# Kernel optimization log

Hardware: AMD Instinct MI355X
Metric: run time of the kernel (lower is better)

The kernel has to match this reference:

```python
import jax, jax.numpy as jnp
import numpy as np

NTRIAL, NNEUR, NT, NT_FULL, NTAU, NLAT, NPAD = 8, 100, 256, 300, 50, 8, 44
LR, JITTER, ZERO_THRESH = 0.2, 1e-3, 1e-5


def setup_inputs() -> dict:
    key = jax.random.key(0)
    k1, k2, k3, k4 = jax.random.split(key, 4)
    Y = jax.random.uniform(k1, (NTRIAL, NNEUR, NT), dtype=jnp.float32)
    raw_input = jax.random.uniform(k2, (NTRIAL, NNEUR, NT_FULL), dtype=jnp.float32)
    kernel = 0.05 * jax.random.normal(k3, (NNEUR, NTAU, NNEUR), dtype=jnp.float32)
    readout = 0.02 * jax.random.normal(k4, (NNEUR, NLAT), dtype=jnp.float32)
    t = jnp.arange(NT, dtype=jnp.float32)
    K = jnp.exp(-(t[:, None] - t[None, :]) ** 2 / (2.0 * 20.0 ** 2))  # RBF latent covariance
    bias = jnp.zeros((), jnp.float32)
    return {"Y": Y, "raw_input": raw_input, "kernel": kernel, "readout": readout,
            "K": K, "bias": bias, "max_iter": 5}


def _conv(raw_input, kernel, npadding):
    # raw_input: (m, i, nt_full); kernel: (i, ntau, j)
    ntrial, ni, nt = raw_input.shape
    zero_pad = jnp.zeros((kernel.shape[0], 1, kernel.shape[2]), kernel.dtype)
    kernel = jnp.concatenate([zero_pad, kernel], axis=1)  # enforce causality
    ntau = kernel.shape[1]
    nn = nt + ntau - 1
    Fx = jnp.fft.fft(raw_input, n=nn, axis=2)[:, :, :, None]   # (m, i, nn, 1)
    Fk = jnp.fft.fft(kernel, n=nn, axis=1)[None]                # (1, i, nn, j)
    G = jnp.fft.ifft(Fx * Fk, axis=2).real
    G = jnp.where(jnp.abs(G) < ZERO_THRESH, 0.0, G)
    G = G[:, :, npadding:nt, :]                                 # (m, i, t, j)
    return jnp.transpose(G, (0, 1, 3, 2)).astype(raw_input.dtype)  # (m, i, j, t)


def _gpfa_poisson_fix_weights(Y, weights, K, bias, max_iter):
    # Y: (m, n, t); weights: (m, n, l, t); K: (t, t)
    ntrial, nneuron, nlatent, nt = weights.shape
    I = jnp.eye(nt, dtype=K.dtype)
    inv_K = jnp.linalg.inv(K + JITTER * I)
    w2 = weights ** 2
    mu0 = jnp.zeros((ntrial, nlatent, nt), K.dtype)
    hess0 = jnp.broadcast_to(inv_K, (ntrial, nlatent, nt, nt)) + jnp.zeros((ntrial, nlatent, 1, 1), K.dtype)

    def step(carry, _):
        mu, hessian, _, _ = carry
        log_lambd = jnp.einsum('mnlt,mlt->mnt', weights, mu) + bias
        hinv = jnp.linalg.inv(hessian)                              # (m, l, t, t)
        dhinv = jnp.diagonal(hinv, axis1=-2, axis2=-1)              # (m, l, t)
        lambd = jnp.exp(log_lambd + 0.5 * jnp.einsum('mlt,mnlt->mnt', dhinv, w2))
        iKh = jnp.einsum('tu,mluv->mltv', inv_K, hinv)              # inv_K @ hessian^{-1}
        muK = jnp.einsum('mlt,tu->mlu', mu, inv_K)
        _, logabs = jnp.linalg.slogdet(iKh)
        loss = (jnp.sum(Y * log_lambd) - jnp.sum(lambd)
                - 0.5 * jnp.sum(muK * mu)
                - 0.5 * jnp.sum(jnp.trace(iKh, axis1=-2, axis2=-1))
                + 0.5 * jnp.sum(logabs) - nt)
        grad = jnp.einsum('mnlt,mnt->mlt', weights, Y - lambd) - muK
        w2l = jnp.einsum('mnlt,mnt->mlt', w2, lambd)                # (m, l, t)
        new_h = -inv_K[None, None] - w2l[..., None] * I             # 4D diagonal add
        mu_upd = jnp.linalg.solve(new_h, grad[..., None])[..., 0]
        return (mu - LR * mu_upd, new_h, lambd, loss), None

    carry0 = (mu0, hess0, jnp.zeros_like(Y), jnp.zeros((), K.dtype))
    (mu, hessian, lambd, loss), _ = jax.lax.scan(step, carry0, None, length=max_iter)
    return mu, lambd, loss


def reference(Y, raw_input, kernel, readout, K, bias, max_iter):
    G = _conv(raw_input, kernel, NPAD)                       # (m, i, j, t)
    weights = jnp.einsum('mijt,il->mjlt', G, readout)        # (m, n=j, l, t)
    mu, lambd, loss = _gpfa_poisson_fix_weights(Y, weights, K, bias, max_iter)
    return mu, lambd, loss
```

## Files before the change

kernel.cpp:

```cpp
#include <hip/hip_runtime.h>

#define NTRIAL 8
#define NNEUR 100
#define NTT 256
#define NT_FULL 300
#define NTAU 50
#define NLAT 8
#define NPAD 44
#define LRATE 0.2f
#define JITTER 0.001f
#define NMAT 64
#define NSLOT 136
#define SPITCH 260
#define NBLKF 35360
#define NBLKF4 8840

__device__ __forceinline__ int bslot(int I, int J){ return ((I*(I+1))>>1) + J; }
__device__ __forceinline__ int rcs(int i, int j){
    return i*16 + ((((j>>2) + (i>>2))&3)<<2) + (j&3);
}
__device__ __forceinline__ int eidx(int I, int J, int i, int j){
    return bslot(I,J)*SPITCH + rcs(i,j);
}
__device__ __forceinline__ int rc4(int i, int q){ return i*4 + ((q + (i>>2))&3); }
__device__ __forceinline__ int f4idx(int I, int J, int i, int q){
    return bslot(I,J)*65 + rc4(i,q);
}
#define DOT4(u,v) (u.x*v.x + u.y*v.y + u.z*v.z + u.w*v.w)

__device__ __forceinline__ void gemmRR(const float4* A, int baseA, const float4* B, int baseB,
                                       int ti, int tj, float acc[4][4]){
    #pragma unroll
    for (int kc = 0; kc < 4; ++kc){
        float4 a0 = A[baseA + rc4(ti+0,kc)];
        float4 a1 = A[baseA + rc4(ti+1,kc)];
        float4 a2 = A[baseA + rc4(ti+2,kc)];
        float4 a3 = A[baseA + rc4(ti+3,kc)];
        float4 b0 = B[baseB + rc4(tj+0,kc)];
        float4 b1 = B[baseB + rc4(tj+1,kc)];
        float4 b2 = B[baseB + rc4(tj+2,kc)];
        float4 b3 = B[baseB + rc4(tj+3,kc)];
        acc[0][0]+=DOT4(a0,b0); acc[0][1]+=DOT4(a0,b1); acc[0][2]+=DOT4(a0,b2); acc[0][3]+=DOT4(a0,b3);
        acc[1][0]+=DOT4(a1,b0); acc[1][1]+=DOT4(a1,b1); acc[1][2]+=DOT4(a1,b2); acc[1][3]+=DOT4(a1,b3);
        acc[2][0]+=DOT4(a2,b0); acc[2][1]+=DOT4(a2,b1); acc[2][2]+=DOT4(a2,b2); acc[2][3]+=DOT4(a2,b3);
        acc[3][0]+=DOT4(a3,b0); acc[3][1]+=DOT4(a3,b1); acc[3][2]+=DOT4(a3,b2); acc[3][3]+=DOT4(a3,b3);
    }
}

__global__ void k_zero(float* mu, float* scal){
    int i = blockIdx.x*256 + threadIdx.x;
    if (i < 16384) mu[i] = 0.f;
    if (i < 64) scal[i] = 0.f;
}

__global__ void k_transpose(const float* __restrict__ kern, float* __restrict__ kt){
    int idx = blockIdx.x*256 + threadIdx.x;
    if (idx >= NNEUR*NTAU*NNEUR) return;
    int i = idx/(NTAU*NNEUR); int rem = idx%(NTAU*NNEUR);
    int tau = rem/NNEUR; int j = rem%NNEUR;
    kt[((size_t)i*NNEUR + j)*NTAU + tau] = kern[idx];
}

__global__ __launch_bounds__(256) void k_conv_weights(const float* __restrict__ raw,
                                                      const float* __restrict__ kt,
                                                      const float* __restrict__ readout,
                                                      float* __restrict__ W){
    int b = blockIdx.x; int m = b / NNEUR; int j = b % NNEUR; int t = threadIdx.x;
    __shared__ float ro[NNEUR*NLAT];
    __shared__ float raw_s[10][NT_FULL];
    __shared__ float kern_s[10][NTAU];
    for (int idx = t; idx < NNEUR*NLAT; idx += 256) ro[idx] = readout[idx];
    float acc[NLAT];
    #pragma unroll
    for (int l = 0; l < NLAT; ++l) acc[l] = 0.f;
    int tmax = min(NTAU, t + NPAD);
    for (int c = 0; c < 10; ++c){
        __syncthreads();
        for (int idx = t; idx < 10*NT_FULL; idx += 256){
            int ii = idx / NT_FULL, tt = idx % NT_FULL;
            raw_s[ii][tt] = raw[((size_t)m*NNEUR + c*10 + ii)*NT_FULL + tt];
        }
        for (int idx = t; idx < 10*NTAU; idx += 256){
            int ii = idx / NTAU, tau = idx % NTAU;
            kern_s[ii][tau] = kt[((size_t)(c*10 + ii)*NNEUR + j)*NTAU + tau];
        }
        __syncthreads();
        for (int ii = 0; ii < 10; ++ii){
            float g = 0.f;
            const float* kr = kern_s[ii];
            const float* rr = raw_s[ii];
            for (int tau = 1; tau <= tmax; ++tau) g += kr[tau-1] * rr[t + NPAD - tau];
            if (fabsf(g) < 1e-5f) g = 0.f;
            const float* rop = &ro[(c*10 + ii)*NLAT];
            #pragma unroll
            for (int l = 0; l < NLAT; ++l) acc[l] += rop[l]*g;
        }
    }
    #pragma unroll
    for (int l = 0; l < NLAT; ++l) W[(((size_t)b)*NLAT + l)*NTT + t] = acc[l];
}

__global__ __launch_bounds__(256) void k_grad2(const float* __restrict__ W, const float* __restrict__ Y,
                                               const float* __restrict__ bias_p,
                                               const float* __restrict__ muIn, const float* __restrict__ diagIn,
                                               float* __restrict__ gradPart, float* __restrict__ w2lPart,
                                               float* __restrict__ lambd, float* __restrict__ scal,
                                               int it0, int it4){
    int blk = blockIdx.x; int m = blk >> 3; int chunk = blk & 7;
    int n0 = chunk*12 + (chunk < 4 ? chunk : 4);
    int cnt = 12 + (chunk < 4 ? 1 : 0);
    int t = threadIdx.x;
    __shared__ float r1[256], r2[256];
    float mul[NLAT], dhl[NLAT];
    #pragma unroll
    for (int l = 0; l < NLAT; ++l){
        mul[l] = muIn[((size_t)(m*NLAT + l))*NTT + t];
        dhl[l] = it0 ? (1.0f + JITTER) : (-diagIn[((size_t)(m*NLAT + l))*NTT + t]);
    }
    float bias = bias_p[0];
    float ga[NLAT], wa[NLAT];
    #pragma unroll
    for (int l = 0; l < NLAT; ++l){ ga[l] = 0.f; wa[l] = 0.f; }
    float yl = 0.f, ls = 0.f;
    for (int n = n0; n < n0 + cnt; ++n){
        size_t base = (((size_t)(m*NNEUR + n))*NLAT)*NTT + t;
        float wl[NLAT];
        float ll = bias, q = 0.f;
        #pragma unroll
        for (int l = 0; l < NLAT; ++l){
            float w = W[base + (size_t)l*NTT];
            wl[l] = w;
            ll += w * mul[l];
            q  += w * w * dhl[l];
        }
        float lam = expf(ll + 0.5f*q);
        float yv = Y[((size_t)(m*NNEUR + n))*NTT + t];
        float d = yv - lam;
        #pragma unroll
        for (int l = 0; l < NLAT; ++l){ ga[l] += wl[l]*d; wa[l] += wl[l]*wl[l]*lam; }
        if (it4){
            lambd[((size_t)(m*NNEUR + n))*NTT + t] = lam;
            yl += yv * ll; ls += lam;
        }
    }
    #pragma unroll
    for (int l = 0; l < NLAT; ++l){
        gradPart[((size_t)((chunk<<6) + m*NLAT + l))*NTT + t] = ga[l];
        w2lPart [((size_t)((chunk<<6) + m*NLAT + l))*NTT + t] = wa[l];
    }
    if (it4){
        r1[t] = yl; r2[t] = ls;
        __syncthreads();
        for (int s = 128; s > 0; s >>= 1){ if (t < s){ r1[t]+=r1[t+s]; r2[t]+=r2[t+s]; } __syncthreads(); }
        if (t == 0){ atomicAdd(&scal[0], r1[0]); atomicAdd(&scal[1], r2[0]); }
    }
}

template<int MODE>
__global__ __launch_bounds__(512) void k_fact(
    const float* __restrict__ Kin,
    const float* __restrict__ invKb,
    const float* __restrict__ gradPart,
    const float* __restrict__ w2lPart,
    const float* __restrict__ muIn,
    float* __restrict__ muOut,
    float* __restrict__ diagOut,
    float* __restrict__ Sout,
    float* __restrict__ scal,
    int it4, int itSlot)
{
    __shared__ float4 P4[NBLKF4];
    __shared__ float4 Bs4[1104];
    __shared__ float4 XinvL4[130];
    __shared__ float dlog[256];
    __shared__ float idg[16];
    float* P     = (float*)P4;
    float* Bsf   = (float*)Bs4;
    float* gs    = Bsf + 3900;
    float* w2ls  = Bsf + 4156;
    float* red   = Bsf;
    float* zp    = Bsf + 512;
    float* muown = dlog;
    const int t = threadIdx.x;
    const int b = blockIdx.x;
    const int g = t>>4, gt = t&15;
    const int ti = (gt>>2)<<2, tj = (gt&3)<<2;
    const int lanebase = t & 48;

    if (MODE == 0){
        if (t < 256){
            int r = t, I = r>>4, i = r&15;
            for (int c = 0; c <= r; ++c)
                P[eidx(I, c>>4, i, c&15)] = Kin[r*256 + c] + ((c==r)?JITTER:0.f);
        }
        __syncthreads();
    } else {
        const float4* G4 = (const float4*)invKb;
        for (int e = t; e < NBLKF4; e += 512) P4[e] = G4[e];
        if (t < 256) muown[t] = muIn[(size_t)b*NTT + t];
        __syncthreads();
        if (t < 256){
            float gg = 0.f, ww = 0.f;
            #pragma unroll
            for (int c = 0; c < 8; ++c){
                gg += gradPart[((size_t)((c<<6) + b))*NTT + t];
                ww += w2lPart [((size_t)((c<<6) + b))*NTT + t];
            }
            int T = t>>4, tb = t&15;
            float mk = 0.f;
            for (int U = 0; U < 16; ++U){
                if (U <= T){
                    #pragma unroll
                    for (int u = 0; u < 16; ++u) mk += muown[U*16+u] * P[eidx(T,U,tb,u)];
                } else {
                    #pragma unroll
                    for (int u = 0; u < 16; ++u) mk += muown[U*16+u] * P[eidx(U,T,u,tb)];
                }
            }
            gs[t]   = gg - mk;
            w2ls[t] = ww;
            red[t]  = mk * muown[t];
        }
        if (it4){
            __syncthreads();
            for (int s = 128; s > 0; s >>= 1){ if (t < s) red[t] += red[t+s]; __syncthreads(); }
            if (t == 0) atomicAdd(&scal[2], red[0]);
        }
        __syncthreads();
        if (t < 256) P[eidx(t>>4, t>>4, t&15, t&15)] += w2ls[t];
        __syncthreads();
    }

    for (int p = 0; p <= 16; ++p){
        const int r = p - 1;
        if (g == 31){
            if (p < 16){
                float x[16];
                if (p > 0){
                    float acc[4][4];
                    #pragma unroll
                    for (int aa=0;aa<4;++aa){acc[aa][0]=0;acc[aa][1]=0;acc[aa][2]=0;acc[aa][3]=0;}
                    gemmRR(P4, bslot(p,r)*65, P4, bslot(p,r)*65, ti, tj, acc);
                    #pragma unroll
                    for (int aa = 0; aa < 4; ++aa){
                        int oi = f4idx(p,p,ti+aa,tj>>2);
                        float4 c = P4[oi];
                        c.x-=acc[aa][0]; c.y-=acc[aa][1]; c.z-=acc[aa][2]; c.w-=acc[aa][3];
                        P4[oi] = c;
                    }
                }
                #pragma unroll
                for (int q = 0; q < 4; ++q){
                    float4 v = P4[f4idx(p,p,gt,q)];
                    x[4*q]=v.x; x[4*q+1]=v.y; x[4*q+2]=v.z; x[4*q+3]=v.w;
                }
                const int i = gt;
                #pragma unroll
                for (int k = 0; k < 16; ++k){
                    float piv = __shfl(x[k], lanebase + k, 64);
                    float d = sqrtf(piv);
                    float dinv = 1.f/d;
                    float lik = (i == k) ? d : x[k]*dinv;
                    if (i >= k) x[k] = lik;
                    #pragma unroll
                    for (int c = k+1; c < 16; ++c){
                        float lck = __shfl(x[k], lanebase + c, 64);
                        if (i >= c) x[c] -= lik*lck;
                    }
                    if (i == k){ idg[k] = dinv; dlog[p*16+k] = d; }
                }
                float col[16];
                #pragma unroll
                for (int ii = 0; ii < 16; ++ii){
                    float s = 0.f;
                    #pragma unroll
                    for (int k = 0; k < 16; ++k){
                        if (k < ii){
                            float lik = __shfl(x[k], lanebase + ii, 64);
                            s += lik * col[k];
                        }
                    }
                    float v = ((gt == ii) ? 1.f : -s) * idg[ii];
                    col[ii] = (gt <= ii) ? v : 0.f;
                }
                #pragma unroll
                for (int q = 0; q < 4; ++q)
                    P4[f4idx(p,p,gt,q)] = make_float4(col[4*q],col[4*q+1],col[4*q+2],col[4*q+3]);
                float* XL = (float*)(XinvL4 + (p&1)*65);
                #pragma unroll
                for (int ii = 0; ii < 16; ++ii) XL[rcs(ii, gt)] = col[ii];
            }
        } else {
            int m16 = 16 - p;
            int ntrail = (p >= 1 && p < 16) ? ((m16*(m16+1))>>1) - 1 : 0;
            int nsm = (p >= 1) ? (p - 1) : 0;
            for (int id = g; id < ntrail + nsm; id += 31){
                if (id < ntrail){
                    int q = id + 1;
                    int di = (int)floorf((sqrtf(8.f*(float)q + 1.f) - 1.f)*0.5f);
                    while (((di+1)*(di+2))>>1 <= q) ++di;
                    while ((di*(di+1))>>1 > q) --di;
                    int dj = q - ((di*(di+1))>>1);
                    int I = p + di, J = p + dj;
                    float acc[4][4];
                    #pragma unroll
                    for (int aa=0;aa<4;++aa){acc[aa][0]=0;acc[aa][1]=0;acc[aa][2]=0;acc[aa][3]=0;}
                    gemmRR(P4, bslot(I,r)*65, P4, bslot(J,r)*65, ti, tj, acc);
                    #pragma unroll
                    for (int aa = 0; aa < 4; ++aa){
                        int oi = f4idx(I,J,ti+aa,tj>>2);
                        float4 c = P4[oi];
                        c.x-=acc[aa][0]; c.y-=acc[aa][1]; c.z-=acc[aa][2]; c.w-=acc[aa][3];
                        P4[oi] = c;
                    }
                } else {
                    int J = id - ntrail;
                    float acc[4][4];
                    #pragma unroll
                    for (int aa=0;aa<4;++aa){acc[aa][0]=0;acc[aa][1]=0;acc[aa][2]=0;acc[aa][3]=0;}
                    gemmRR(Bs4, J*65, XinvL4, (r&1)*65, ti, tj, acc);
                    #pragma unroll
                    for (int aa = 0; aa < 4; ++aa)
                        P4[f4idx(r,J,ti+aa,tj>>2)] =
                            make_float4(-acc[aa][0],-acc[aa][1],-acc[aa][2],-acc[aa][3]);
                }
            }
        }
        __syncthreads();
        if (p == 16) break;
        if (g < 2*p){
            int J = g>>1, half = g&1;
            float acc[4][4];
            #pragma unroll
            for (int aa=0;aa<4;++aa){acc[aa][0]=0;acc[aa][1]=0;acc[aa][2]=0;acc[aa][3]=0;}
            for (int K = J + half; K < p; K += 2)
                gemmRR(P4, bslot(p,K)*65, P4, bslot(K,J)*65, ti, tj, acc);
            #pragma unroll
            for (int aa = 0; aa < 4; ++aa){
                #pragma unroll
                for (int bb = 0; bb < 4; ++bb)
                    acc[aa][bb] += __shfl_xor(acc[aa][bb], 16, 64);
            }
            if (half == 0){
                float* BJ = Bsf + J*260;
                #pragma unroll
                for (int aa = 0; aa < 4; ++aa)
                    #pragma unroll
                    for (int bb = 0; bb < 4; ++bb)
                        BJ[rcs(tj+bb, ti+aa)] = acc[aa][bb];
            }
        } else {
            int I = p + 1 + (g - 2*p);
            if (I < 16){
                float acc[4][4];
                #pragma unroll
                for (int aa=0;aa<4;++aa){acc[aa][0]=0;acc[aa][1]=0;acc[aa][2]=0;acc[aa][3]=0;}
                gemmRR(P4, bslot(I,p)*65, XinvL4, (p&1)*65, ti, tj, acc);
                #pragma unroll
                for (int aa = 0; aa < 4; ++aa)
                    P4[f4idx(I,p,ti+aa,tj>>2)] =
                        make_float4(acc[aa][0],acc[aa][1],acc[aa][2],acc[aa][3]);
            }
        }
        __syncthreads();
    }

    if (MODE == 0){
        red[t] = (t < 256) ? 2.f*logf(dlog[t]) : 0.f;
        __syncthreads();
        for (int s = 128; s > 0; s >>= 1){ if (t < s) red[t] += red[t+s]; __syncthreads(); }
        if (t == 0) scal[20] = red[0];
        float4* SO = (float4*)Sout;
        for (int e = t; e < NBLKF4; e += 512) SO[e] = P4[e];
        return;
    } else {
        float dsum = 0.f;
        if (t < 256){
            const int J0 = t>>4, j0 = t&15;
            for (int I = J0; I < 16; ++I){
                #pragma unroll
                for (int q = 0; q < 4; ++q){
                    float4 v = P4[f4idx(I,J0,j0,q)];
                    dsum += v.x*v.x + v.y*v.y + v.z*v.z + v.w*v.w;
                }
            }
            diagOut[(size_t)b*NTT + t] = dsum;
            const int Ir = t>>4, rb = t&15;
            float z = 0.f;
            for (int J = 0; J <= Ir; ++J){
                #pragma unroll
                for (int j = 0; j < 16; ++j) z += P[eidx(Ir,J,j,rb)]*gs[J*16+j];
            }
            zp[t] = z;
        }
        __syncthreads();
        if (t < 256){
            const int J0 = t>>4, j0 = t&15;
            float u = 0.f;
            for (int I = J0; I < 16; ++I){
                #pragma unroll
                for (int q = 0; q < 4; ++q){
                    float4 v = P4[f4idx(I,J0,j0,q)];
                    const float* zz = &zp[I*16 + 4*q];
                    u += v.x*zz[0] + v.y*zz[1] + v.z*zz[2] + v.w*zz[3];
                }
            }
            muOut[(size_t)b*NTT + t] = muIn[(size_t)b*NTT + t] + LRATE*u;
            red[t]       = w2ls[t]*dsum;
            red[256 + t] = 2.f*logf(dlog[t]);
        }
        __syncthreads();
        for (int s = 128; s > 0; s >>= 1){
            if (t < s){ red[t] += red[t+s]; red[256+t] += red[256+t+s]; }
            __syncthreads();
        }
        if (t == 0){
            atomicAdd(&scal[8 + itSlot],  red[0] - 256.f);
            atomicAdd(&scal[24 + itSlot], -scal[20] - red[256]);
        }
    }
}

__global__ __launch_bounds__(256) void k_syrk(const float* __restrict__ S,
                                              float* __restrict__ invKb){
    int sidx = blockIdx.x;
    int I = (int)floorf((sqrtf(8.f*(float)sidx + 1.f) - 1.f)*0.5f);
    while (((I+1)*(I+2))>>1 <= sidx) ++I;
    while ((I*(I+1))>>1 > sidx) --I;
    int J = sidx - ((I*(I+1))>>1);
    int t = threadIdx.x; int i = t>>4, j = t&15;
    __shared__ float4 sA[64], sB[64];
    const float4* S4 = (const float4*)S;
    float s = 0.f;
    for (int R = I; R < 16; ++R){
        __syncthreads();
        if (t < 64) sA[t] = S4[bslot(R,I)*65 + t];
        else if (t < 128) sB[t-64] = S4[bslot(R,J)*65 + t-64];
        __syncthreads();
        #pragma unroll
        for (int q = 0; q < 4; ++q){
            float4 a = sA[rc4(i,q)];
            float4 c = sB[rc4(j,q)];
            s += a.x*c.x + a.y*c.y + a.z*c.z + a.w*c.w;
        }
    }
    invKb[eidx(I,J,i,j)] = s;
}

__global__ void k_loss(const float* __restrict__ scal, float* __restrict__ out_loss){
    out_loss[0] = scal[0] - scal[1] - 0.5f*scal[2] - 0.5f*scal[8+3] + 0.5f*scal[24+3] - 256.f;
}

__global__ void k_gather(const float* __restrict__ mu, const float* __restrict__ lambd, float* __restrict__ out){
    int idx = blockIdx.x*256 + threadIdx.x;
    if (idx < 16384) out[idx] = mu[idx];
    else if (idx < 16384 + 204800) out[idx] = lambd[idx - 16384];
}

extern "C" void kernel_launch(void* const* d_in, const int* in_sizes, int n_in,
                              void* d_out, int out_size, void* d_ws, size_t ws_size,
                              hipStream_t stream){
    (void)in_sizes; (void)n_in; (void)out_size; (void)ws_size;
    const float* Y       = (const float*)d_in[0];
    const float* raw     = (const float*)d_in[1];
    const float* kern    = (const float*)d_in[2];
    const float* readout = (const float*)d_in[3];
    const float* K       = (const float*)d_in[4];
    const float* bias    = (const float*)d_in[5];
    float* out = (float*)d_out;
    float* ws  = (float*)d_ws;

    float* invKb    = ws;
    float* Sblk     = invKb + NBLKF;
    float* W        = Sblk + NBLKF;
    float* muA      = W + 1638400;
    float* muB      = muA + 16384;
    float* lambd    = muB + 16384;
    float* diagA    = lambd + 204800;
    float* diagB    = diagA + 16384;
    float* gradPart = diagB + 16384;
    float* w2lPart  = gradPart + 131072;
    float* scal     = w2lPart + 131072;
    float* kt       = scal + 64;

    k_zero<<<64, 256, 0, stream>>>(muA, scal);
    k_transpose<<<(NNEUR*NTAU*NNEUR + 255)/256, 256, 0, stream>>>(kern, kt);
    k_conv_weights<<<NTRIAL*NNEUR, 256, 0, stream>>>(raw, kt, readout, W);

    k_fact<0><<<1, 512, 0, stream>>>(K, nullptr, nullptr, nullptr, nullptr,
                                     nullptr, nullptr, Sblk, scal, 0, 0);
    k_syrk<<<NSLOT, 256, 0, stream>>>(Sblk, invKb);

    for (int it = 0; it < 5; ++it){
        const float* muI = (it & 1) ? muB : muA;
        float*       muO = (it & 1) ? muA : muB;
        const float* dI  = (it & 1) ? diagB : diagA;
        float*       dO  = (it & 1) ? diagA : diagB;
        int it0 = (it == 0) ? 1 : 0;
        int it4 = (it == 4) ? 1 : 0;
        k_grad2<<<64, 256, 0, stream>>>(W, Y, bias, muI, dI, gradPart, w2lPart,
                                        lambd, scal, it0, it4);
        k_fact<1><<<NMAT, 512, 0, stream>>>(nullptr, invKb, gradPart, w2lPart, muI,
                                            muO, dO, nullptr, scal, it4, it);
    }
    k_loss<<<1, 1, 0, stream>>>(scal, out + 16384 + 204800);
    k_gather<<<864, 256, 0, stream>>>(muB, lambd, out);
}
```

Baseline: 1.695 ms.

## Factor scaled K-based matrix per trial instead of inverse-K Hessian

Drops the upfront Cholesky of K and the SYRK that formed inv(K). Each iteration now factors I + D^½ K D^½ directly from K, using a fused TRSM that writes a per-matrix C buffer in global memory. The Newton update, the diagonal and the mu·K⁻¹ term are rebuilt through Woodbury-style identities, with a new carried vector v replacing the inv(K)·mu product. This removes the serial single-block factorization and the dense inverse-K algebra, at the cost of extra global traffic for a 256x256 buffer per matrix and different numerical behaviour.

After: 1.592 ms. -6.1%, faster.

```diff
diff --git a/kernel.cpp b/kernel.cpp
--- a/kernel.cpp
+++ b/kernel.cpp
@@ -12,19 +12,24 @@
 #define NMAT 64
 #define NSLOT 136
 #define SPITCH 260
-#define NBLKF 35360
 #define NBLKF4 8840
 
 __device__ __forceinline__ int bslot(int I, int J){ return ((I*(I+1))>>1) + J; }
 __device__ __forceinline__ int rcs(int i, int j){
     return i*16 + ((((j>>2) + (i>>2))&3)<<2) + (j&3);
 }
-__device__ __forceinline__ int eidx(int I, int J, int i, int j){
-    return bslot(I,J)*SPITCH + rcs(i,j);
-}
 __device__ __forceinline__ int rc4(int i, int q){ return i*4 + ((q + (i>>2))&3); }
 __device__ __forceinline__ int f4idx(int I, int J, int i, int q){
     return bslot(I,J)*65 + rc4(i,q);
+}
+__device__ __forceinline__ float4 f4fma(float s, float4 v, float4 a){
+    a.x += s*v.x; a.y += s*v.y; a.z += s*v.z; a.w += s*v.w; return a;
+}
+__device__ __forceinline__ void sdecode(int s, int& I, int& J){
+    int i = (int)floorf((sqrtf(8.f*(float)s + 1.f) - 1.f)*0.5f);
+    while (((i+1)*(i+2))>>1 <= s) ++i;
+    while ((i*(i+1))>>1 > s) --i;
+    I = i; J = s - ((i*(i+1))>>1);
 }
 #define DOT4(u,v) (u.x*v.x + u.y*v.y + u.z*v.z + u.w*v.w)
 
@@ -47,9 +52,9 @@
     }
 }
 
-__global__ void k_zero(float* mu, float* scal){
+__global__ void k_zero(float* mu, float* v, float* scal){
     int i = blockIdx.x*256 + threadIdx.x;
-    if (i < 16384) mu[i] = 0.f;
+    if (i < 16384){ mu[i] = 0.f; v[i] = 0.f; }
     if (i < 64) scal[i] = 0.f;
 }
 
@@ -156,156 +161,224 @@
     }
 }
 
-template<int MODE>
-__global__ __launch_bounds__(512) void k_fact(
-    const float* __restrict__ Kin,
-    const float* __restrict__ invKb,
+__device__ __forceinline__ void trsm_tile(
+    int r, int j, int half,
+    const float* __restrict__ Kg, float* __restrict__ Cb,
+    const float4* P4, const float4* XinvL4,
+    const float* dsc, float* colnorm,
+    int gt, int ti, int tj, int lanebase)
+{
+    float4 t0 = make_float4(0.f,0.f,0.f,0.f), t1 = t0, t2 = t0, t3 = t0;
+    const float4* C4 = (const float4*)Cb;
+    const int cchunk = (j<<2) + (tj>>2);
+    for (int K = half; K < r; K += 2){
+        const int ab = bslot(r,K)*65;
+        #pragma unroll
+        for (int kc = 0; kc < 4; ++kc){
+            float4 a0 = P4[ab + rc4(ti+0,kc)];
+            float4 a1 = P4[ab + rc4(ti+1,kc)];
+            float4 a2 = P4[ab + rc4(ti+2,kc)];
+            float4 a3 = P4[ab + rc4(ti+3,kc)];
+            const int cr = (((K<<4) + (kc<<2))<<6) + cchunk;
+            float4 c0 = C4[cr], c1 = C4[cr+64], c2 = C4[cr+128], c3 = C4[cr+192];
+            t0 = f4fma(-a0.x,c0, f4fma(-a0.y,c1, f4fma(-a0.z,c2, f4fma(-a0.w,c3, t0))));
+            t1 = f4fma(-a1.x,c0, f4fma(-a1.y,c1, f4fma(-a1.z,c2, f4fma(-a1.w,c3, t1))));
+            t2 = f4fma(-a2.x,c0, f4fma(-a2.y,c1, f4fma(-a2.z,c2, f4fma(-a2.w,c3, t2))));
+            t3 = f4fma(-a3.x,c0, f4fma(-a3.y,c1, f4fma(-a3.z,c2, f4fma(-a3.w,c3, t3))));
+        }
+    }
+    if (half == 0){
+        const float4* K4 = (const float4*)Kg;
+        #pragma unroll
+        for (int a = 0; a < 4; ++a){
+            int row = (r<<4) + ti + a;
+            float4 kv = K4[row*64 + cchunk];
+            int dcol = row - ((j<<4) + tj);
+            if (dcol >= 0 && dcol < 4) ((float*)&kv)[dcol] += JITTER;
+            float s = dsc[row];
+            if      (a == 0) t0 = f4fma(s, kv, t0);
+            else if (a == 1) t1 = f4fma(s, kv, t1);
+            else if (a == 2) t2 = f4fma(s, kv, t2);
+            else             t3 = f4fma(s, kv, t3);
+        }
+    }
+    t0.x += __shfl_xor(t0.x,16,64); t0.y += __shfl_xor(t0.y,16,64); t0.z += __shfl_xor(t0.z,16,64); t0.w += __shfl_xor(t0.w,16,64);
+    t1.x += __shfl_xor(t1.x,16,64); t1.y += __shfl_xor(t1.y,16,64); t1.z += __shfl_xor(t1.z,16,64); t1.w += __shfl_xor(t1.w,16,64);
+    t2.x += __shfl_xor(t2.x,16,64); t2.y += __shfl_xor(t2.y,16,64); t2.z += __shfl_xor(t2.z,16,64); t2.w += __shfl_xor(t2.w,16,64);
+    t3.x += __shfl_xor(t3.x,16,64); t3.y += __shfl_xor(t3.y,16,64); t3.z += __shfl_xor(t3.z,16,64); t3.w += __shfl_xor(t3.w,16,64);
+    if (half) return;
+    const float4* XB = XinvL4 + (r&1)*65;
+    float4 o0 = make_float4(0.f,0.f,0.f,0.f), o1 = o0, o2 = o0, o3 = o0;
+    #pragma unroll
+    for (int kc = 0; kc < 4; ++kc){
+        int src = lanebase + (kc<<2) + (gt&3);
+        float4 v0, v1, v2, v3;
+        v0.x=__shfl(t0.x,src,64); v0.y=__shfl(t0.y,src,64); v0.z=__shfl(t0.z,src,64); v0.w=__shfl(t0.w,src,64);
+        v1.x=__shfl(t1.x,src,64); v1.y=__shfl(t1.y,src,64); v1.z=__shfl(t1.z,src,64); v1.w=__shfl(t1.w,src,64);
+        v2.x=__shfl(t2.x,src,64); v2.y=__shfl(t2.y,src,64); v2.z=__shfl(t2.z,src,64); v2.w=__shfl(t2.w,src,64);
+        v3.x=__shfl(t3.x,src,64); v3.y=__shfl(t3.y,src,64); v3.z=__shfl(t3.z,src,64); v3.w=__shfl(t3.w,src,64);
+        float4 x0 = XB[rc4(ti+0,kc)], x1 = XB[rc4(ti+1,kc)], x2 = XB[rc4(ti+2,kc)], x3 = XB[rc4(ti+3,kc)];
+        o0 = f4fma(x0.x,v0, f4fma(x0.y,v1, f4fma(x0.z,v2, f4fma(x0.w,v3, o0))));
+        o1 = f4fma(x1.x,v0, f4fma(x1.y,v1, f4fma(x1.z,v2, f4fma(x1.w,v3, o1))));
+        o2 = f4fma(x2.x,v0, f4fma(x2.y,v1, f4fma(x2.z,v2, f4fma(x2.w,v3, o2))));
+        o3 = f4fma(x3.x,v0, f4fma(x3.y,v1, f4fma(x3.z,v2, f4fma(x3.w,v3, o3))));
+    }
+    float4 cn;
+    cn.x = o0.x*o0.x + o1.x*o1.x + o2.x*o2.x + o3.x*o3.x;
+    cn.y = o0.y*o0.y + o1.y*o1.y + o2.y*o2.y + o3.y*o3.y;
+    cn.z = o0.z*o0.z + o1.z*o1.z + o2.z*o2.z + o3.z*o3.z;
+    cn.w = o0.w*o0.w + o1.w*o1.w + o2.w*o2.w + o3.w*o3.w;
+    cn.x += __shfl_xor(cn.x,4,64); cn.y += __shfl_xor(cn.y,4,64); cn.z += __shfl_xor(cn.z,4,64); cn.w += __shfl_xor(cn.w,4,64);
+    cn.x += __shfl_xor(cn.x,8,64); cn.y += __shfl_xor(cn.y,8,64); cn.z += __shfl_xor(cn.z,8,64); cn.w += __shfl_xor(cn.w,8,64);
+    if (gt < 4){
+        int cb = (j<<4) + (gt<<2);
+        colnorm[cb+0] += cn.x; colnorm[cb+1] += cn.y; colnorm[cb+2] += cn.z; colnorm[cb+3] += cn.w;
+    }
+    float4* C4w = (float4*)Cb;
+    const int wr = (((r<<4)+ti)<<6) + cchunk;
+    C4w[wr]       = o0;
+    C4w[wr + 64]  = o1;
+    C4w[wr + 128] = o2;
+    C4w[wr + 192] = o3;
+}
+
+__global__ __launch_bounds__(512) void k_fact2(
+    const float* __restrict__ Kg,
     const float* __restrict__ gradPart,
     const float* __restrict__ w2lPart,
     const float* __restrict__ muIn,
+    const float* __restrict__ vIn,
     float* __restrict__ muOut,
+    float* __restrict__ vOut,
     float* __restrict__ diagOut,
-    float* __restrict__ Sout,
+    float* __restrict__ Cbuf,
     float* __restrict__ scal,
     int it4, int itSlot)
 {
     __shared__ float4 P4[NBLKF4];
-    __shared__ float4 Bs4[1104];
     __shared__ float4 XinvL4[130];
     __shared__ float dlog[256];
     __shared__ float idg[16];
-    float* P     = (float*)P4;
-    float* Bsf   = (float*)Bs4;
-    float* gs    = Bsf + 3900;
-    float* w2ls  = Bsf + 4156;
-    float* red   = Bsf;
-    float* zp    = Bsf + 512;
-    float* muown = dlog;
+    __shared__ __align__(16) float gs[256];
+    __shared__ float w2ls[256], dsc[256], colnorm[256];
+    __shared__ float scr[1024];
+    __shared__ float sldM;
     const int t = threadIdx.x;
     const int b = blockIdx.x;
     const int g = t>>4, gt = t&15;
     const int ti = (gt>>2)<<2, tj = (gt&3)<<2;
     const int lanebase = t & 48;
-
-    if (MODE == 0){
-        if (t < 256){
-            int r = t, I = r>>4, i = r&15;
-            for (int c = 0; c <= r; ++c)
-                P[eidx(I, c>>4, i, c&15)] = Kin[r*256 + c] + ((c==r)?JITTER:0.f);
-        }
-        __syncthreads();
-    } else {
-        const float4* G4 = (const float4*)invKb;
-        for (int e = t; e < NBLKF4; e += 512) P4[e] = G4[e];
-        if (t < 256) muown[t] = muIn[(size_t)b*NTT + t];
-        __syncthreads();
-        if (t < 256){
-            float gg = 0.f, ww = 0.f;
+    float* Cb = Cbuf + (size_t)b*65536;
+
+    float muin_r = 0.f, vin_r = 0.f;
+    if (t < 256){
+        float gg = 0.f, ww = 0.f;
+        #pragma unroll
+        for (int c = 0; c < 8; ++c){
+            gg += gradPart[(((size_t)((c<<6) + b))<<8) + t];
+            ww += w2lPart [(((size_t)((c<<6) + b))<<8) + t];
+        }
+        muin_r = muIn[((size_t)b<<8) + t];
+        vin_r  = vIn [((size_t)b<<8) + t];
+        w2ls[t] = ww; dsc[t] = sqrtf(ww);
+        gs[t] = gg - vin_r;
+        colnorm[t] = 0.f;
+    }
+    __syncthreads();
+    {
+        const float4* K4 = (const float4*)Kg;
+        for (int s = g; s < NSLOT; s += 32){
+            int I, J; sdecode(s, I, J);
+            int row = (I<<4) + gt;
+            float dr = dsc[row];
             #pragma unroll
-            for (int c = 0; c < 8; ++c){
-                gg += gradPart[((size_t)((c<<6) + b))*NTT + t];
-                ww += w2lPart [((size_t)((c<<6) + b))*NTT + t];
-            }
-            int T = t>>4, tb = t&15;
-            float mk = 0.f;
-            for (int U = 0; U < 16; ++U){
-                if (U <= T){
-                    #pragma unroll
-                    for (int u = 0; u < 16; ++u) mk += muown[U*16+u] * P[eidx(T,U,tb,u)];
-                } else {
-                    #pragma unroll
-                    for (int u = 0; u < 16; ++u) mk += muown[U*16+u] * P[eidx(U,T,u,tb)];
+            for (int q = 0; q < 4; ++q){
+                float4 kv = K4[row*64 + (J<<2) + q];
+                int cb = (J<<4) + (q<<2);
+                kv.x *= dr*dsc[cb+0]; kv.y *= dr*dsc[cb+1]; kv.z *= dr*dsc[cb+2]; kv.w *= dr*dsc[cb+3];
+                if (I == J){
+                    int dcol = gt - (q<<2);
+                    if (dcol >= 0 && dcol < 4) ((float*)&kv)[dcol] += 1.f + dr*dr*JITTER;
                 }
-            }
-            gs[t]   = gg - mk;
-            w2ls[t] = ww;
-            red[t]  = mk * muown[t];
-        }
-        if (it4){
+                P4[s*65 + rc4(gt,q)] = kv;
+            }
+        }
+    }
+    __syncthreads();
+
+    for (int p = 0; p <= 16; ++p){
+        if (p == 16){
+            trsm_tile(15, g>>1, g&1, Kg, Cb, P4, XinvL4, dsc, colnorm, gt, ti, tj, lanebase);
             __syncthreads();
-            for (int s = 128; s > 0; s >>= 1){ if (t < s) red[t] += red[t+s]; __syncthreads(); }
-            if (t == 0) atomicAdd(&scal[2], red[0]);
-        }
-        __syncthreads();
-        if (t < 256) P[eidx(t>>4, t>>4, t&15, t&15)] += w2ls[t];
-        __syncthreads();
-    }
-
-    for (int p = 0; p <= 16; ++p){
-        const int r = p - 1;
+            break;
+        }
         if (g == 31){
-            if (p < 16){
-                float x[16];
-                if (p > 0){
-                    float acc[4][4];
-                    #pragma unroll
-                    for (int aa=0;aa<4;++aa){acc[aa][0]=0;acc[aa][1]=0;acc[aa][2]=0;acc[aa][3]=0;}
-                    gemmRR(P4, bslot(p,r)*65, P4, bslot(p,r)*65, ti, tj, acc);
-                    #pragma unroll
-                    for (int aa = 0; aa < 4; ++aa){
-                        int oi = f4idx(p,p,ti+aa,tj>>2);
-                        float4 c = P4[oi];
-                        c.x-=acc[aa][0]; c.y-=acc[aa][1]; c.z-=acc[aa][2]; c.w-=acc[aa][3];
-                        P4[oi] = c;
+            float x[16];
+            if (p > 0){
+                float acc[4][4];
+                #pragma unroll
+                for (int aa=0;aa<4;++aa){acc[aa][0]=0;acc[aa][1]=0;acc[aa][2]=0;acc[aa][3]=0;}
+                gemmRR(P4, bslot(p,p-1)*65, P4, bslot(p,p-1)*65, ti, tj, acc);
+                #pragma unroll
+                for (int aa = 0; aa < 4; ++aa){
+                    int oi = f4idx(p,p,ti+aa,tj>>2);
+                    float4 c = P4[oi];
+                    c.x-=acc[aa][0]; c.y-=acc[aa][1]; c.z-=acc[aa][2]; c.w-=acc[aa][3];
+                    P4[oi] = c;
+                }
+            }
+            #pragma unroll
+            for (int q = 0; q < 4; ++q){
+                float4 v = P4[f4idx(p,p,gt,q)];
+                x[4*q]=v.x; x[4*q+1]=v.y; x[4*q+2]=v.z; x[4*q+3]=v.w;
+            }
+            const int i = gt;
+            #pragma unroll
+            for (int k = 0; k < 16; ++k){
+                float piv = __shfl(x[k], lanebase + k, 64);
+                float d = sqrtf(piv);
+                float dinv = 1.f/d;
+                float lik = (i == k) ? d : x[k]*dinv;
+                if (i >= k) x[k] = lik;
+                #pragma unroll
+                for (int c = k+1; c < 16; ++c){
+                    float lck = __shfl(x[k], lanebase + c, 64);
+                    if (i >= c) x[c] -= lik*lck;
+                }
+                if (i == k){ idg[k] = dinv; dlog[p*16+k] = d; }
+            }
+            float col[16];
+            #pragma unroll
+            for (int ii = 0; ii < 16; ++ii){
+                float s = 0.f;
+                #pragma unroll
+                for (int k = 0; k < 16; ++k){
+                    if (k < ii){
+                        float lik = __shfl(x[k], lanebase + ii, 64);
+                        s += lik * col[k];
                     }
                 }
-                #pragma unroll
-                for (int q = 0; q < 4; ++q){
-                    float4 v = P4[f4idx(p,p,gt,q)];
-                    x[4*q]=v.x; x[4*q+1]=v.y; x[4*q+2]=v.z; x[4*q+3]=v.w;
-                }
-                const int i = gt;
-                #pragma unroll
-                for (int k = 0; k < 16; ++k){
-                    float piv = __shfl(x[k], lanebase + k, 64);
-                    float d = sqrtf(piv);
-                    float dinv = 1.f/d;
-                    float lik = (i == k) ? d : x[k]*dinv;
-                    if (i >= k) x[k] = lik;
-                    #pragma unroll
-                    for (int c = k+1; c < 16; ++c){
-                        float lck = __shfl(x[k], lanebase + c, 64);
-                        if (i >= c) x[c] -= lik*lck;
-                    }
-                    if (i == k){ idg[k] = dinv; dlog[p*16+k] = d; }
-                }
-                float col[16];
-                #pragma unroll
-                for (int ii = 0; ii < 16; ++ii){
-                    float s = 0.f;
-                    #pragma unroll
-                    for (int k = 0; k < 16; ++k){
-                        if (k < ii){
-                            float lik = __shfl(x[k], lanebase + ii, 64);
-                            s += lik * col[k];
-                        }
-                    }
-                    float v = ((gt == ii) ? 1.f : -s) * idg[ii];
-                    col[ii] = (gt <= ii) ? v : 0.f;
-                }
-                #pragma unroll
-                for (int q = 0; q < 4; ++q)
-                    P4[f4idx(p,p,gt,q)] = make_float4(col[4*q],col[4*q+1],col[4*q+2],col[4*q+3]);
-                float* XL = (float*)(XinvL4 + (p&1)*65);
-                #pragma unroll
-                for (int ii = 0; ii < 16; ++ii) XL[rcs(ii, gt)] = col[ii];
-            }
-        } else {
+                float v = ((gt == ii) ? 1.f : -s) * idg[ii];
+                col[ii] = (gt <= ii) ? v : 0.f;
+            }
+            float* XL = (float*)(XinvL4 + (p&1)*65);
+            #pragma unroll
+            for (int ii = 0; ii < 16; ++ii) XL[rcs(ii, gt)] = col[ii];
+        } else if (g < 28){
+            int ntrsm = (p >= 1) ? 16 : 0;
             int m16 = 16 - p;
-            int ntrail = (p >= 1 && p < 16) ? ((m16*(m16+1))>>1) - 1 : 0;
-            int nsm = (p >= 1) ? (p - 1) : 0;
-            for (int id = g; id < ntrail + nsm; id += 31){
-                if (id < ntrail){
-                    int q = id + 1;
-                    int di = (int)floorf((sqrtf(8.f*(float)q + 1.f) - 1.f)*0.5f);
-                    while (((di+1)*(di+2))>>1 <= q) ++di;
-                    while ((di*(di+1))>>1 > q) --di;
-                    int dj = q - ((di*(di+1))>>1);
+            int ntrail = (p >= 1) ? ((m16*(m16+1))>>1) - 1 : 0;
+            for (int id = g; id < ntrsm + ntrail; id += 28){
+                if (id < ntrsm){
+                    trsm_tile(p-1, id>>1, id&1, Kg, Cb, P4, XinvL4, dsc, colnorm, gt, ti, tj, lanebase);
+                } else {
+                    int q = id - ntrsm + 1;
+                    int di, dj; sdecode(q, di, dj);
                     int I = p + di, J = p + dj;
                     float acc[4][4];
                     #pragma unroll
                     for (int aa=0;aa<4;++aa){acc[aa][0]=0;acc[aa][1]=0;acc[aa][2]=0;acc[aa][3]=0;}
-                    gemmRR(P4, bslot(I,r)*65, P4, bslot(J,r)*65, ti, tj, acc);
+                    gemmRR(P4, bslot(I,p-1)*65, P4, bslot(J,p-1)*65, ti, tj, acc);
                     #pragma unroll
                     for (int aa = 0; aa < 4; ++aa){
                         int oi = f4idx(I,J,ti+aa,tj>>2);
@@ -313,45 +386,15 @@
                         c.x-=acc[aa][0]; c.y-=acc[aa][1]; c.z-=acc[aa][2]; c.w-=acc[aa][3];
                         P4[oi] = c;
                     }
-                } else {
-                    int J = id - ntrail;
-                    float acc[4][4];
-                    #pragma unroll
-                    for (int aa=0;aa<4;++aa){acc[aa][0]=0;acc[aa][1]=0;acc[aa][2]=0;acc[aa][3]=0;}
-                    gemmRR(Bs4, J*65, XinvL4, (r&1)*65, ti, tj, acc);
-                    #pragma unroll
-                    for (int aa = 0; aa < 4; ++aa)
-                        P4[f4idx(r,J,ti+aa,tj>>2)] =
-                            make_float4(-acc[aa][0],-acc[aa][1],-acc[aa][2],-acc[aa][3]);
                 }
             }
         }
         __syncthreads();
-        if (p == 16) break;
-        if (g < 2*p){
-            int J = g>>1, half = g&1;
-            float acc[4][4];
-            #pragma unroll
-            for (int aa=0;aa<4;++aa){acc[aa][0]=0;acc[aa][1]=0;acc[aa][2]=0;acc[aa][3]=0;}
-            for (int K = J + half; K < p; K += 2)
-                gemmRR(P4, bslot(p,K)*65, P4, bslot(K,J)*65, ti, tj, acc);
-            #pragma unroll
-            for (int aa = 0; aa < 4; ++aa){
-                #pragma unroll
-                for (int bb = 0; bb < 4; ++bb)
-                    acc[aa][bb] += __shfl_xor(acc[aa][bb], 16, 64);
-            }
-            if (half == 0){
-                float* BJ = Bsf + J*260;
-                #pragma unroll
-                for (int aa = 0; aa < 4; ++aa)
-                    #pragma unroll
-                    for (int bb = 0; bb < 4; ++bb)
-                        BJ[rcs(tj+bb, ti+aa)] = acc[aa][bb];
-            }
-        } else {
-            int I = p + 1 + (g - 2*p);
-            if (I < 16){
+        if (p >= 1 && g < 16){
+            trsm_tile(p-1, 8 + (g>>1), g&1, Kg, Cb, P4, XinvL4, dsc, colnorm, gt, ti, tj, lanebase);
+        } else if (g >= 16 && g < 31){
+            for (int id = g - 16; id < 15 - p; id += 15){
+                int I = p + 1 + id;
                 float acc[4][4];
                 #pragma unroll
                 for (int aa=0;aa<4;++aa){acc[aa][0]=0;acc[aa][1]=0;acc[aa][2]=0;acc[aa][3]=0;}
@@ -365,86 +408,63 @@
         __syncthreads();
     }
 
-    if (MODE == 0){
-        red[t] = (t < 256) ? 2.f*logf(dlog[t]) : 0.f;
+    scr[t] = (t < 256) ? 2.f*logf(dlog[t]) : 0.f;
+    __syncthreads();
+    for (int s = 256; s > 0; s >>= 1){ if (t < s) scr[t] += scr[t+s]; __syncthreads(); }
+    if (t == 0) sldM = scr[0];
+    __syncthreads();
+    {
+        int t2 = t & 255, hf = t >> 8;
+        float acc = 0.f;
+        const float* Kr = Kg + (size_t)hf*128*256 + t2;
+        for (int u = 0; u < 128; ++u) acc += gs[hf*128 + u]*Kr[(size_t)u*256];
+        scr[(hf<<8) + t2] = acc;
+    }
+    __syncthreads();
+    float* hv = (float*)XinvL4;
+    if (t < 256) hv[t] = scr[t] + scr[256+t];
+    {
+        int t2 = t & 255, hf = t >> 8;
+        const float4* Crow = ((const float4*)Cb) + (size_t)t2*64;
+        const float4* g4 = (const float4*)gs;
+        float acc = 0.f;
+        for (int q = hf*32; q < hf*32 + 32; ++q){
+            float4 c = Crow[q], gq = g4[q];
+            acc += c.x*gq.x + c.y*gq.y + c.z*gq.z + c.w*gq.w;
+        }
+        scr[512 + (hf<<8) + t2] = acc;
+    }
+    __syncthreads();
+    if (t < 256) dlog[t] = scr[512+t] + scr[768+t];
+    __syncthreads();
+    {
+        int t2 = t & 255, hf = t >> 8;
+        float acc = 0.f;
+        const float* Cp = Cb + (size_t)hf*128*256 + t2;
+        for (int i = 0; i < 128; ++i) acc += Cp[(size_t)i*256]*dlog[hf*128 + i];
+        scr[(hf<<8) + t2] = acc;
+    }
+    __syncthreads();
+    if (t < 256){
+        float ct = scr[t] + scr[256+t];
+        float uval = hv[t] + JITTER*gs[t] - ct;
+        float diagv = Kg[(size_t)t*257] + JITTER - colnorm[t];
+        diagOut[((size_t)b<<8) + t] = diagv;
+        muOut[((size_t)b<<8) + t] = muin_r + LRATE*uval;
+        vOut [((size_t)b<<8) + t] = vin_r + LRATE*(gs[t] - w2ls[t]*uval);
+        scr[t]     = w2ls[t]*diagv;
+        scr[256+t] = it4 ? (vin_r*muin_r) : 0.f;
+    }
+    __syncthreads();
+    for (int s = 128; s > 0; s >>= 1){
+        if (t < s){ scr[t] += scr[t+s]; scr[256+t] += scr[256+t+s]; }
         __syncthreads();
-        for (int s = 128; s > 0; s >>= 1){ if (t < s) red[t] += red[t+s]; __syncthreads(); }
-        if (t == 0) scal[20] = red[0];
-        float4* SO = (float4*)Sout;
-        for (int e = t; e < NBLKF4; e += 512) SO[e] = P4[e];
-        return;
-    } else {
-        float dsum = 0.f;
-        if (t < 256){
-            const int J0 = t>>4, j0 = t&15;
-            for (int I = J0; I < 16; ++I){
-                #pragma unroll
-                for (int q = 0; q < 4; ++q){
-                    float4 v = P4[f4idx(I,J0,j0,q)];
-                    dsum += v.x*v.x + v.y*v.y + v.z*v.z + v.w*v.w;
-                }
-            }
-            diagOut[(size_t)b*NTT + t] = dsum;
-            const int Ir = t>>4, rb = t&15;
-            float z = 0.f;
-            for (int J = 0; J <= Ir; ++J){
-                #pragma unroll
-                for (int j = 0; j < 16; ++j) z += P[eidx(Ir,J,j,rb)]*gs[J*16+j];
-            }
-            zp[t] = z;
-        }
-        __syncthreads();
-        if (t < 256){
-            const int J0 = t>>4, j0 = t&15;
-            float u = 0.f;
-            for (int I = J0; I < 16; ++I){
-                #pragma unroll
-                for (int q = 0; q < 4; ++q){
-                    float4 v = P4[f4idx(I,J0,j0,q)];
-                    const float* zz = &zp[I*16 + 4*q];
-                    u += v.x*zz[0] + v.y*zz[1] + v.z*zz[2] + v.w*zz[3];
-                }
-            }
-            muOut[(size_t)b*NTT + t] = muIn[(size_t)b*NTT + t] + LRATE*u;
-            red[t]       = w2ls[t]*dsum;
-            red[256 + t] = 2.f*logf(dlog[t]);
-        }
-        __syncthreads();
-        for (int s = 128; s > 0; s >>= 1){
-            if (t < s){ red[t] += red[t+s]; red[256+t] += red[256+t+s]; }
-            __syncthreads();
-        }
-        if (t == 0){
-            atomicAdd(&scal[8 + itSlot],  red[0] - 256.f);
-            atomicAdd(&scal[24 + itSlot], -scal[20] - red[256]);
-        }
-    }
-}
-
-__global__ __launch_bounds__(256) void k_syrk(const float* __restrict__ S,
-                                              float* __restrict__ invKb){
-    int sidx = blockIdx.x;
-    int I = (int)floorf((sqrtf(8.f*(float)sidx + 1.f) - 1.f)*0.5f);
-    while (((I+1)*(I+2))>>1 <= sidx) ++I;
-    while ((I*(I+1))>>1 > sidx) --I;
-    int J = sidx - ((I*(I+1))>>1);
-    int t = threadIdx.x; int i = t>>4, j = t&15;
-    __shared__ float4 sA[64], sB[64];
-    const float4* S4 = (const float4*)S;
-    float s = 0.f;
-    for (int R = I; R < 16; ++R){
-        __syncthreads();
-        if (t < 64) sA[t] = S4[bslot(R,I)*65 + t];
-        else if (t < 128) sB[t-64] = S4[bslot(R,J)*65 + t-64];
-        __syncthreads();
-        #pragma unroll
-        for (int q = 0; q < 4; ++q){
-            float4 a = sA[rc4(i,q)];
-            float4 c = sB[rc4(j,q)];
-            s += a.x*c.x + a.y*c.y + a.z*c.z + a.w*c.w;
-        }
-    }
-    invKb[eidx(I,J,i,j)] = s;
+    }
+    if (t == 0){
+        atomicAdd(&scal[8 + itSlot],  scr[0] - 256.f);
+        atomicAdd(&scal[24 + itSlot], -sldM);
+        if (it4) atomicAdd(&scal[2], scr[256]);
+    }
 }
 
 __global__ void k_loss(const float* __restrict__ scal, float* __restrict__ out_loss){
@@ -470,38 +490,37 @@
     float* out = (float*)d_out;
     float* ws  = (float*)d_ws;
 
-    float* invKb    = ws;
-    float* Sblk     = invKb + NBLKF;
-    float* W        = Sblk + NBLKF;
-    float* muA      = W + 1638400;
+    float* W        = ws;
+    float* Cbuf     = W + 1638400;
+    float* muA      = Cbuf + 4194304;
     float* muB      = muA + 16384;
-    float* lambd    = muB + 16384;
-    float* diagA    = lambd + 204800;
+    float* vA       = muB + 16384;
+    float* vB       = vA + 16384;
+    float* diagA    = vB + 16384;
     float* diagB    = diagA + 16384;
     float* gradPart = diagB + 16384;
     float* w2lPart  = gradPart + 131072;
-    float* scal     = w2lPart + 131072;
+    float* lambd    = w2lPart + 131072;
+    float* scal     = lambd + 204800;
     float* kt       = scal + 64;
 
-    k_zero<<<64, 256, 0, stream>>>(muA, scal);
+    k_zero<<<64, 256, 0, stream>>>(muA, vA, scal);
     k_transpose<<<(NNEUR*NTAU*NNEUR + 255)/256, 256, 0, stream>>>(kern, kt);
     k_conv_weights<<<NTRIAL*NNEUR, 256, 0, stream>>>(raw, kt, readout, W);
-
-    k_fact<0><<<1, 512, 0, stream>>>(K, nullptr, nullptr, nullptr, nullptr,
-                                     nullptr, nullptr, Sblk, scal, 0, 0);
-    k_syrk<<<NSLOT, 256, 0, stream>>>(Sblk, invKb);
 
     for (int it = 0; it < 5; ++it){
         const float* muI = (it & 1) ? muB : muA;
         float*       muO = (it & 1) ? muA : muB;
+        const float* vI  = (it & 1) ? vB : vA;
+        float*       vO  = (it & 1) ? vA : vB;
         const float* dI  = (it & 1) ? diagB : diagA;
         float*       dO  = (it & 1) ? diagA : diagB;
         int it0 = (it == 0) ? 1 : 0;
         int it4 = (it == 4) ? 1 : 0;
         k_grad2<<<64, 256, 0, stream>>>(W, Y, bias, muI, dI, gradPart, w2lPart,
                                         lambd, scal, it0, it4);
-        k_fact<1><<<NMAT, 512, 0, stream>>>(nullptr, invKb, gradPart, w2lPart, muI,
-                                            muO, dO, nullptr, scal, it4, it);
+        k_fact2<<<NMAT, 512, 0, stream>>>(K, gradPart, w2lPart, muI, vI,
+                                          muO, vO, dO, Cbuf, scal, it4, it);
     }
     k_loss<<<1, 1, 0, stream>>>(scal, out + 16384 + 204800);
     k_gather<<<864, 256, 0, stream>>>(muB, lambd, out);
```
